# Optimization experiments

Hardware: AMD Instinct MI355X
Metric: run time of the kernel (lower is better)

Reference implementation:

```python
import jax, jax.numpy as jnp
import numpy as np

N_NODES = 100000
N_EDGES = 1600000
D_IN = 128
D_HID = 128
LATENT = 64
N_GRAPHS = 512


def setup_inputs() -> dict:
    key = jax.random.key(0)
    ks = jax.random.split(key, 10)
    x = jax.random.normal(ks[0], (N_NODES, D_IN), dtype=jnp.float32)
    edge_index = jax.random.randint(ks[1], (2, N_EDGES), 0, N_NODES, dtype=jnp.int64)
    batch = jnp.sort(jax.random.randint(ks[2], (N_NODES,), 0, N_GRAPHS, dtype=jnp.int64))
    def lin(k, fan_in, fan_out):
        return jax.random.normal(k, (fan_in, fan_out), dtype=jnp.float32) / np.sqrt(fan_in)
    W1 = lin(ks[3], D_IN, D_HID); b1 = jnp.zeros((D_HID,), jnp.float32)
    W2 = lin(ks[4], D_HID, D_HID); b2 = jnp.zeros((D_HID,), jnp.float32)
    W3 = lin(ks[5], D_HID, 2 * LATENT); b3 = jnp.zeros((2 * LATENT,), jnp.float32)
    return {"x": x, "edge_index": edge_index, "batch": batch,
            "W1": W1, "b1": b1, "W2": W2, "b2": b2, "W3": W3, "b3": b3}


def _gcn_norm(edge_index, n_nodes):
    # PyG GCNConv default: add self-loops, symmetric normalization
    loop = jnp.arange(n_nodes, dtype=edge_index.dtype)
    src = jnp.concatenate([edge_index[0], loop])
    dst = jnp.concatenate([edge_index[1], loop])
    deg = jax.ops.segment_sum(jnp.ones_like(dst, dtype=jnp.float32), dst,
                              num_segments=n_nodes)
    dinv = jnp.where(deg > 0, jax.lax.rsqrt(deg), 0.0)
    norm = dinv[src] * dinv[dst]  # [E + N]
    return src, dst, norm


def _gcn_conv(x, W, b, src, dst, norm, n_nodes):
    h = x @ W                               # [N, d_out]
    msg = h[src] * norm[:, None]            # gather + scale, [E+N, d_out]
    agg = jax.ops.segment_sum(msg, dst, num_segments=n_nodes)
    return agg + b


def reference(x, edge_index, batch, W1, b1, W2, b2, W3, b3):
    n = x.shape[0]
    src, dst, norm = _gcn_norm(edge_index, n)
    h = jax.nn.relu(_gcn_conv(x, W1, b1, src, dst, norm, n))
    h = jax.nn.relu(_gcn_conv(h, W2, b2, src, dst, norm, n))
    h = _gcn_conv(h, W3, b3, src, dst, norm, n)
    # scatter_mean over batch ids -> [num_graphs, 2*latent]
    cnt = jax.ops.segment_sum(jnp.ones((n,), jnp.float32), batch,
                              num_segments=N_GRAPHS)
    summed = jax.ops.segment_sum(h, batch, num_segments=N_GRAPHS)
    return summed / jnp.maximum(cnt, 1.0)[:, None]
```

## Files before the change

kernel.cpp:

```cpp
#include <hip/hip_runtime.h>
#include <stdint.h>

typedef unsigned short u16;
typedef unsigned int   u32;

#define N_NODES  100000
#define N_EDGES  1600000
#define DFEAT    128
#define N_GRAPHS 512

#define NBKT   391
#define EPB    8192
#define NBLK_E 196
#define LBUF   8192

typedef float f32x4 __attribute__((ext_vector_type(4)));
typedef short s16x8 __attribute__((ext_vector_type(8)));

__device__ __forceinline__ float bflo(u32 u) { return __uint_as_float(u << 16); }
__device__ __forceinline__ float bfhi(u32 u) { return __uint_as_float(u & 0xffff0000u); }
__device__ __forceinline__ u16 f2bf(float f) {
  u32 u = __float_as_uint(f);
  return (u16)((u + 0x7fffu + ((u >> 16) & 1u)) >> 16);
}
__device__ __forceinline__ u32 pack2(float f0, float f1) {
  return (u32)f2bf(f0) | ((u32)f2bf(f1) << 16);
}

__device__ __forceinline__ int ld_src(const int* ei, int m, int e) {
  return m ? ei[2 * e] : ei[e];
}
__device__ __forceinline__ int ld_dst(const int* ei, int m, int e) {
  return m ? ei[2 * (N_EDGES + e)] : ei[N_EDGES + e];
}

__device__ __forceinline__ int detect_m_block(const int* __restrict__ ei, int* sm) {
  int t = threadIdx.x;
  if (t < 64) {
    int v = ei[2 * t + 1];
    unsigned long long b = __ballot(v != 0);
    if (t == 0) *sm = (b == 0ull) ? 1 : 0;
  }
  __syncthreads();
  return *sm;
}

__global__ __launch_bounds__(256) void histA_k(const int* __restrict__ ei,
                                               int* __restrict__ ghist,
                                               const float* __restrict__ W1,
                                               const float* __restrict__ W2,
                                               const float* __restrict__ W3,
                                               u16* __restrict__ T1, u16* __restrict__ T2,
                                               u16* __restrict__ T3, int* __restrict__ flag) {
  int t = threadIdx.x, b = blockIdx.x;
  if (b >= NBLK_E) {
    int r = b - NBLK_E;
    if (r < 3) {
      const float* W = (r == 0) ? W1 : (r == 1) ? W2 : W3;
      u16* T         = (r == 0) ? T1 : (r == 1) ? T2 : T3;
      for (int i = t; i < DFEAT * DFEAT; i += 256) {
        int n = i >> 7, k = i & 127;
        T[i] = f2bf(W[k * DFEAT + n]);
      }
    } else {
      if (t < 64) {
        int v = ei[2 * t + 1];
        unsigned long long mm = __ballot(v != 0);
        if (t == 0) *flag = (mm == 0ull) ? 1 : 0;
      }
    }
    return;
  }
  __shared__ int sm;
  __shared__ int hist[NBKT];
  int m = detect_m_block(ei, &sm);
  for (int i = t; i < NBKT; i += 256) hist[i] = 0;
  __syncthreads();
  int e0 = b * EPB;
#pragma unroll
  for (int p = 0; p < EPB / 256; p++) {
    int e = e0 + p * 256 + t;
    if (e < N_EDGES) atomicAdd(&hist[ld_dst(ei, m, e) >> 8], 1);
  }
  __syncthreads();
  for (int i = t; i < NBKT; i += 256) ghist[b * NBKT + i] = hist[i];
}

__global__ __launch_bounds__(256) void scanB1_k(int* __restrict__ ghist,
                                                int* __restrict__ gtot) {
  __shared__ int ts[256];
  int t = threadIdx.x, k = blockIdx.x;
  int v = (t < NBLK_E) ? ghist[t * NBKT + k] : 0;
  ts[t] = v;
  for (int off = 1; off < 256; off <<= 1) {
    __syncthreads(); int add = (t >= off) ? ts[t - off] : 0;
    __syncthreads(); ts[t] += add;
  }
  __syncthreads();
  if (t < NBLK_E) ghist[t * NBKT + k] = ts[t] - v;
  if (t == 255) gtot[k] = ts[255];
}

__device__ __forceinline__ void scan_gtot_block(const int* __restrict__ gtot,
                                                int* bb, int* sc) {
  int t = threadIdx.x;
  int v0 = gtot[t];
  sc[t] = v0;
  for (int off = 1; off < 256; off <<= 1) {
    __syncthreads(); int add = (t >= off) ? sc[t - off] : 0;
    __syncthreads(); sc[t] += add;
  }
  __syncthreads();
  bb[t] = sc[t] - v0;
  int base256 = sc[255];
  __syncthreads();
  int v1 = (t < NBKT - 256) ? gtot[256 + t] : 0;
  sc[t] = v1;
  for (int off = 1; off < 256; off <<= 1) {
    __syncthreads(); int add = (t >= off) ? sc[t - off] : 0;
    __syncthreads(); sc[t] += add;
  }
  __syncthreads();
  if (t < NBKT - 256) bb[256 + t] = base256 + sc[t] - v1;
  if (t == 0) bb[NBKT] = N_EDGES;
  __syncthreads();
}

__global__ __launch_bounds__(256) void scatterC_k(const int* __restrict__ ei,
                                                  const int* __restrict__ obase,
                                                  const int* __restrict__ gtot,
                                                  u32* __restrict__ colpk) {
  __shared__ int sm;
  __shared__ int cur[NBKT];
  __shared__ int bb[NBKT + 1];
  __shared__ int sc[256];
  int t = threadIdx.x, b = blockIdx.x;
  int m = detect_m_block(ei, &sm);
  scan_gtot_block(gtot, bb, sc);
  for (int i = t; i < NBKT; i += 256) cur[i] = bb[i] + obase[b * NBKT + i];
  __syncthreads();
  int e0 = b * EPB;
#pragma unroll
  for (int p = 0; p < EPB / 256; p++) {
    int e = e0 + p * 256 + t;
    if (e < N_EDGES) {
      int d = ld_dst(ei, m, e);
      int s = ld_src(ei, m, e);
      int pos = atomicAdd(&cur[d >> 8], 1);
      colpk[pos] = (u32)s | ((u32)(d & 255) << 24);
    }
  }
}

__global__ __launch_bounds__(256) void fillD_k(const int* __restrict__ gtot,
                                               const u32* __restrict__ colpk,
                                               int* __restrict__ colarr,
                                               int* __restrict__ rowptr,
                                               float* __restrict__ dinv) {
  __shared__ int hist[256];
  __shared__ int cur[256];
  __shared__ int lbuf[LBUF];
  __shared__ int bb[NBKT + 1];
  __shared__ int sc[256];
  int t = threadIdx.x, b = blockIdx.x;
  scan_gtot_block(gtot, bb, sc);
  int base = bb[b], end = bb[b + 1], cnt = end - base;
  hist[t] = 0;
  __syncthreads();
  for (int i = t; i < cnt; i += 256) atomicAdd(&hist[colpk[base + i] >> 24], 1);
  __syncthreads();
  int c = hist[t];
  cur[t] = c;
  for (int off = 1; off < 256; off <<= 1) {
    __syncthreads(); int add = (t >= off) ? cur[t - off] : 0;
    __syncthreads(); cur[t] += add;
  }
  __syncthreads();
  int excl = cur[t] - c;
  int node = b * 256 + t;
  if (node < N_NODES) {
    rowptr[node] = base + excl;
    dinv[node] = rsqrtf((float)(c + 1));
  }
  if (b == NBKT - 1 && t == 0) rowptr[N_NODES] = N_EDGES;
  __syncthreads();
  cur[t] = excl;
  __syncthreads();
  for (int i = t; i < cnt; i += 256) {
    u32 v = colpk[base + i];
    int slot = atomicAdd(&cur[v >> 24], 1);
    if (slot < LBUF) lbuf[slot] = (int)(v & 0x00FFFFFFu);
  }
  __syncthreads();
  for (int i = t; i < cnt; i += 256) colarr[base + i] = lbuf[i];
}

#define LP 136

__global__ __launch_bounds__(256, 1) void gemm_scale_k(const void* __restrict__ Xv,
                                                       int x_is_f32,
                                                       const u16* __restrict__ Wt,
                                                       const float* __restrict__ dinv,
                                                       u16* __restrict__ Y, int nrows) {
  __shared__ u16 sX[128 * LP];
  __shared__ u16 sW[128 * LP];
  int tid = threadIdx.x;
  int r0 = blockIdx.x * 128;

  for (int c = tid; c < 2048; c += 256) {
    int row = c >> 4, off = (c & 15) * 8;
    *(uint4*)(&sW[row * LP + off]) = *(const uint4*)(Wt + row * DFEAT + off);
  }
  if (x_is_f32) {
    const float* Xf = (const float*)Xv;
    for (int c = tid; c < 2048; c += 256) {
      int row = c >> 4, off = (c & 15) * 8;
      int grow = r0 + row;
      uint4 o = make_uint4(0, 0, 0, 0);
      if (grow < nrows) {
        const float* px = Xf + (size_t)grow * DFEAT + off;
        float4 v0 = *(const float4*)px;
        float4 v1 = *(const float4*)(px + 4);
        o.x = pack2(v0.x, v0.y); o.y = pack2(v0.z, v0.w);
        o.z = pack2(v1.x, v1.y); o.w = pack2(v1.z, v1.w);
      }
      *(uint4*)(&sX[row * LP + off]) = o;
    }
  } else {
    const u16* Xb = (const u16*)Xv;
    for (int c = tid; c < 2048; c += 256) {
      int row = c >> 4, off = (c & 15) * 8;
      int grow = r0 + row;
      uint4 v = make_uint4(0, 0, 0, 0);
      if (grow < nrows) v = *(const uint4*)(Xb + (size_t)grow * DFEAT + off);
      *(uint4*)(&sX[row * LP + off]) = v;
    }
  }
  __syncthreads();

  int wave = tid >> 6, lane = tid & 63;
  int q = lane >> 4, r = lane & 15;
  int wr0 = wave * 32;

  f32x4 acc[2][8];
#pragma unroll
  for (int m = 0; m < 2; m++)
#pragma unroll
    for (int i = 0; i < 8; i++) acc[m][i] = (f32x4){0.f, 0.f, 0.f, 0.f};

#pragma unroll
  for (int kk = 0; kk < 4; kk++) {
    int k0 = kk * 32;
    s16x8 a0 = *(const s16x8*)(&sX[(wr0 + r) * LP + k0 + q * 8]);
    s16x8 a1 = *(const s16x8*)(&sX[(wr0 + 16 + r) * LP + k0 + q * 8]);
#pragma unroll
    for (int nt = 0; nt < 8; nt++) {
      s16x8 b = *(const s16x8*)(&sW[(nt * 16 + r) * LP + k0 + q * 8]);
      acc[0][nt] = __builtin_amdgcn_mfma_f32_16x16x32_bf16(a0, b, acc[0][nt], 0, 0, 0);
      acc[1][nt] = __builtin_amdgcn_mfma_f32_16x16x32_bf16(a1, b, acc[1][nt], 0, 0, 0);
    }
  }

#pragma unroll
  for (int m = 0; m < 2; m++) {
#pragma unroll
    for (int i = 0; i < 4; i++) {
      int grow = r0 + wr0 + m * 16 + q * 4 + i;
      if (grow < nrows) {
        float dv = dinv[grow];
#pragma unroll
        for (int nt = 0; nt < 8; nt++) {
          Y[(size_t)grow * DFEAT + nt * 16 + r] = f2bf(acc[m][nt][i] * dv);
        }
      }
    }
  }
}

struct Acc8 {
  float a0, a1, a2, a3, a4, a5, a6, a7;
  __device__ __forceinline__ void add(uint4 v) {
    a0 += bflo(v.x); a1 += bfhi(v.x); a2 += bflo(v.y); a3 += bfhi(v.y);
    a4 += bflo(v.z); a5 += bfhi(v.z); a6 += bflo(v.w); a7 += bfhi(v.w);
  }
};

__global__ __launch_bounds__(256) void agg_k(const u32* __restrict__ HS,
                                             const float* __restrict__ dinv,
                                             const int* __restrict__ rowptr,
                                             const int* __restrict__ colidx,
                                             const float* __restrict__ bias,
                                             u32* __restrict__ OUT, int do_relu) {
  int t = threadIdx.x;
  int node = blockIdx.x * 16 + (t >> 4);
  int fp = t & 15;

  int s = rowptr[node], e = rowptr[node + 1];

  Acc8 A;
  uint4 v = *(const uint4*)(HS + (size_t)node * 64 + fp * 4);
  A.a0 = bflo(v.x); A.a1 = bfhi(v.x); A.a2 = bflo(v.y); A.a3 = bfhi(v.y);
  A.a4 = bflo(v.z); A.a5 = bfhi(v.z); A.a6 = bflo(v.w); A.a7 = bfhi(v.w);

  int j = s;
  for (; j + 4 <= e; j += 4) {
    int i0 = colidx[j], i1 = colidx[j + 1], i2 = colidx[j + 2], i3 = colidx[j + 3];
    uint4 w0 = *(const uint4*)(HS + (size_t)i0 * 64 + fp * 4);
    uint4 w1 = *(const uint4*)(HS + (size_t)i1 * 64 + fp * 4);
    uint4 w2 = *(const uint4*)(HS + (size_t)i2 * 64 + fp * 4);
    uint4 w3 = *(const uint4*)(HS + (size_t)i3 * 64 + fp * 4);
    A.add(w0); A.add(w1); A.add(w2); A.add(w3);
  }
  for (; j < e; j++) {
    int i0 = colidx[j];
    uint4 w0 = *(const uint4*)(HS + (size_t)i0 * 64 + fp * 4);
    A.add(w0);
  }

  float dv = dinv[node];
  float4 b0 = *(const float4*)(bias + fp * 8);
  float4 b1 = *(const float4*)(bias + fp * 8 + 4);
  float r0 = A.a0 * dv + b0.x, r1 = A.a1 * dv + b0.y;
  float r2 = A.a2 * dv + b0.z, r3 = A.a3 * dv + b0.w;
  float r4 = A.a4 * dv + b1.x, r5 = A.a5 * dv + b1.y;
  float r6 = A.a6 * dv + b1.z, r7 = A.a7 * dv + b1.w;
  if (do_relu) {
    r0 = fmaxf(r0, 0.f); r1 = fmaxf(r1, 0.f); r2 = fmaxf(r2, 0.f); r3 = fmaxf(r3, 0.f);
    r4 = fmaxf(r4, 0.f); r5 = fmaxf(r5, 0.f); r6 = fmaxf(r6, 0.f); r7 = fmaxf(r7, 0.f);
  }
  uint4 o;
  o.x = pack2(r0, r1); o.y = pack2(r2, r3); o.z = pack2(r4, r5); o.w = pack2(r6, r7);
  *(uint4*)(OUT + (size_t)node * 64 + fp * 4) = o;
}

__device__ __forceinline__ int lower_bound_i(const int* a, int n, int key, int shift) {
  int lo = 0, hi = n;
  while (lo < hi) {
    int mid = (lo + hi) >> 1;
    if (a[mid << shift] < key) lo = mid + 1; else hi = mid;
  }
  return lo;
}

__global__ __launch_bounds__(256) void pool_k(const u32* __restrict__ H,
                                              const int* __restrict__ batch,
                                              const int* __restrict__ flag,
                                              float* __restrict__ OUT) {
  int g = blockIdx.x;
  int m = *flag;
  int lo = lower_bound_i(batch, N_NODES, g, m);
  int hi = lower_bound_i(batch, N_NODES, g + 1, m);
  int cnt = hi - lo;
  int d2 = threadIdx.x & 63;
  int half = threadIdx.x >> 6;
  float a0 = 0.f, a1 = 0.f;
  for (int row = lo + half; row < hi; row += 4) {
    u32 v = H[(size_t)row * 64 + d2];
    a0 += bflo(v); a1 += bfhi(v);
  }
  __shared__ float red0[256], red1[256];
  red0[threadIdx.x] = a0; red1[threadIdx.x] = a1;
  __syncthreads();
  if (threadIdx.x < 64) {
    float s0 = red0[d2] + red0[d2 + 64] + red0[d2 + 128] + red0[d2 + 192];
    float s1 = red1[d2] + red1[d2 + 64] + red1[d2 + 128] + red1[d2 + 192];
    float inv = 1.0f / fmaxf((float)cnt, 1.0f);
    OUT[g * DFEAT + 2 * d2]     = s0 * inv;
    OUT[g * DFEAT + 2 * d2 + 1] = s1 * inv;
  }
}


extern "C" void kernel_launch(void* const* d_in, const int* in_sizes, int n_in,
                              void* d_out, int out_size, void* d_ws, size_t ws_size,
                              hipStream_t stream) {
  const float* x   = (const float*)d_in[0];
  const int* ei    = (const int*)d_in[1];
  const int* batch = (const int*)d_in[2];
  const float* W1  = (const float*)d_in[3];
  const float* b1  = (const float*)d_in[4];
  const float* W2  = (const float*)d_in[5];
  const float* b2  = (const float*)d_in[6];
  const float* W3  = (const float*)d_in[7];
  const float* b3  = (const float*)d_in[8];
  float* out = (float*)d_out;

  char* p = (char*)d_ws;
  size_t off = 0;
  auto carve = [&](size_t bytes) -> void* {
    void* q = p + off;
    off = (off + bytes + 255) & ~(size_t)255;
    return q;
  };
  int*   flag   = (int*)carve(256);
  int*   ghist  = (int*)carve((size_t)NBLK_E * NBKT * 4);
  int*   gtot   = (int*)carve(NBKT * 4);
  int*   rowptr = (int*)carve((N_NODES + 1) * 4);
  float* dinv   = (float*)carve(N_NODES * 4);
  u32*   colpk  = (u32*)carve((size_t)N_EDGES * 4);
  int*   colarr = (int*)carve((size_t)N_EDGES * 4);
  u16*   Wt1    = (u16*)carve(DFEAT * DFEAT * 2);
  u16*   Wt2    = (u16*)carve(DFEAT * DFEAT * 2);
  u16*   Wt3    = (u16*)carve(DFEAT * DFEAT * 2);
  u32*   bufA   = (u32*)carve((size_t)N_NODES * 64 * 4);
  u32*   bufB   = (u32*)carve((size_t)N_NODES * 64 * 4);
  (void)ws_size;

  histA_k<<<NBLK_E + 4, 256, 0, stream>>>(ei, ghist, W1, W2, W3, Wt1, Wt2, Wt3, flag);
  scanB1_k<<<NBKT, 256, 0, stream>>>(ghist, gtot);
  scatterC_k<<<NBLK_E, 256, 0, stream>>>(ei, ghist, gtot, colpk);
  fillD_k<<<NBKT, 256, 0, stream>>>(gtot, colpk, colarr, rowptr, dinv);

  const int GB = (N_NODES + 127) / 128;
  const int AB = N_NODES / 16;

  gemm_scale_k<<<GB, 256, 0, stream>>>((const void*)x, 1, Wt1, dinv, (u16*)bufA, N_NODES);
  agg_k<<<AB, 256, 0, stream>>>(bufA, dinv, rowptr, colarr, b1, bufB, 1);
  gemm_scale_k<<<GB, 256, 0, stream>>>((const void*)bufB, 0, Wt2, dinv, (u16*)bufA, N_NODES);
  agg_k<<<AB, 256, 0, stream>>>(bufA, dinv, rowptr, colarr, b2, bufB, 1);
  gemm_scale_k<<<GB, 256, 0, stream>>>((const void*)bufB, 0, Wt3, dinv, (u16*)bufA, N_NODES);
  agg_k<<<AB, 256, 0, stream>>>(bufA, dinv, rowptr, colarr, b3, bufB, 0);
  pool_k<<<N_GRAPHS, 256, 0, stream>>>(bufB, batch, flag, out);
}
```

Before: 405.9 us.

## Fuse first GEMM with graph build and fuse aggregation with next-layer GEMM

The first-layer GEMM (with on-the-fly W1 transpose and bf16 conversion) now runs in the same launch as the edge histogram and weight prep, so it no longer waits on the CSR build. Because dinv is not yet known at that point, layer-1 aggregation applies the per-source dinv scaling inside the gather. Each aggregation is fused with the following layer's GEMM on a 16-row tile via MFMA, with weights read straight from global memory. The scan kernel is removed: scatter and fill blocks each re-sum the histogram columns redundantly. This cuts launches and intermediate round-trips, at the cost of redundant histogram reads, extra dinv gathers in layer 1, and a small-tile GEMM with poor weight reuse.

Result: slower. 436.9 us (+7.6%).

```diff
diff --git a/kernel.cpp b/kernel.cpp
--- a/kernel.cpp
+++ b/kernel.cpp
@@ -13,6 +13,7 @@
 #define EPB    8192
 #define NBLK_E 196
 #define LBUF   8192
+#define GB     782
 
 typedef float f32x4 __attribute__((ext_vector_type(4)));
 typedef short s16x8 __attribute__((ext_vector_type(8)));
@@ -45,66 +46,120 @@
   return *sm;
 }
 
-__global__ __launch_bounds__(256) void histA_k(const int* __restrict__ ei,
-                                               int* __restrict__ ghist,
-                                               const float* __restrict__ W1,
-                                               const float* __restrict__ W2,
-                                               const float* __restrict__ W3,
-                                               u16* __restrict__ T1, u16* __restrict__ T2,
-                                               u16* __restrict__ T3, int* __restrict__ flag) {
-  int t = threadIdx.x, b = blockIdx.x;
-  if (b >= NBLK_E) {
-    int r = b - NBLK_E;
-    if (r < 3) {
-      const float* W = (r == 0) ? W1 : (r == 1) ? W2 : W3;
-      u16* T         = (r == 0) ? T1 : (r == 1) ? T2 : T3;
-      for (int i = t; i < DFEAT * DFEAT; i += 256) {
-        int n = i >> 7, k = i & 127;
-        T[i] = f2bf(W[k * DFEAT + n]);
+#define LP 136
+
+__global__ __launch_bounds__(256) void mega_k(const float* __restrict__ x,
+                                              const int* __restrict__ ei,
+                                              int* __restrict__ ghist,
+                                              const float* __restrict__ W1,
+                                              const float* __restrict__ W2,
+                                              const float* __restrict__ W3,
+                                              u16* __restrict__ T2, u16* __restrict__ T3,
+                                              int* __restrict__ flag,
+                                              u16* __restrict__ Y) {
+  __shared__ u16 sX[128 * LP];
+  __shared__ u16 sW[128 * LP];
+  __shared__ int hist[NBKT];
+  __shared__ int sm;
+  int tid = threadIdx.x, b = blockIdx.x;
+
+  if (b < GB) {
+    int r0 = b * 128;
+    for (int c = tid; c < 2048; c += 256) {
+      int n = c & 127, k0 = (c >> 7) * 8;
+#pragma unroll
+      for (int j = 0; j < 8; j++)
+        sW[n * LP + k0 + j] = f2bf(W1[(size_t)(k0 + j) * DFEAT + n]);
+    }
+    for (int c = tid; c < 2048; c += 256) {
+      int row = c >> 4, off = (c & 15) * 8;
+      int grow = r0 + row;
+      uint4 o = make_uint4(0, 0, 0, 0);
+      if (grow < N_NODES) {
+        const float* px = x + (size_t)grow * DFEAT + off;
+        float4 v0 = *(const float4*)px;
+        float4 v1 = *(const float4*)(px + 4);
+        o.x = pack2(v0.x, v0.y); o.y = pack2(v0.z, v0.w);
+        o.z = pack2(v1.x, v1.y); o.w = pack2(v1.z, v1.w);
       }
-    } else {
-      if (t < 64) {
-        int v = ei[2 * t + 1];
-        unsigned long long mm = __ballot(v != 0);
-        if (t == 0) *flag = (mm == 0ull) ? 1 : 0;
+      *(uint4*)(&sX[row * LP + off]) = o;
+    }
+    __syncthreads();
+
+    int wave = tid >> 6, lane = tid & 63;
+    int q = lane >> 4, r = lane & 15;
+    int wr0 = wave * 32;
+
+    f32x4 acc[2][8];
+#pragma unroll
+    for (int m = 0; m < 2; m++)
+#pragma unroll
+      for (int i = 0; i < 8; i++) acc[m][i] = (f32x4){0.f, 0.f, 0.f, 0.f};
+
+#pragma unroll
+    for (int kk = 0; kk < 4; kk++) {
+      int k0 = kk * 32;
+      s16x8 a0 = *(const s16x8*)(&sX[(wr0 + r) * LP + k0 + q * 8]);
+      s16x8 a1 = *(const s16x8*)(&sX[(wr0 + 16 + r) * LP + k0 + q * 8]);
+#pragma unroll
+      for (int nt = 0; nt < 8; nt++) {
+        s16x8 bb = *(const s16x8*)(&sW[(nt * 16 + r) * LP + k0 + q * 8]);
+        acc[0][nt] = __builtin_amdgcn_mfma_f32_16x16x32_bf16(a0, bb, acc[0][nt], 0, 0, 0);
+        acc[1][nt] = __builtin_amdgcn_mfma_f32_16x16x32_bf16(a1, bb, acc[1][nt], 0, 0, 0);
       }
     }
+
+#pragma unroll
+    for (int m = 0; m < 2; m++) {
+#pragma unroll
+      for (int i = 0; i < 4; i++) {
+        int grow = r0 + wr0 + m * 16 + q * 4 + i;
+        if (grow < N_NODES) {
+#pragma unroll
+          for (int nt = 0; nt < 8; nt++)
+            Y[(size_t)grow * DFEAT + nt * 16 + r] = f2bf(acc[m][nt][i]);
+        }
+      }
+    }
     return;
   }
-  __shared__ int sm;
-  __shared__ int hist[NBKT];
-  int m = detect_m_block(ei, &sm);
-  for (int i = t; i < NBKT; i += 256) hist[i] = 0;
-  __syncthreads();
-  int e0 = b * EPB;
-#pragma unroll
-  for (int p = 0; p < EPB / 256; p++) {
-    int e = e0 + p * 256 + t;
-    if (e < N_EDGES) atomicAdd(&hist[ld_dst(ei, m, e) >> 8], 1);
-  }
-  __syncthreads();
-  for (int i = t; i < NBKT; i += 256) ghist[b * NBKT + i] = hist[i];
-}
-
-__global__ __launch_bounds__(256) void scanB1_k(int* __restrict__ ghist,
-                                                int* __restrict__ gtot) {
-  __shared__ int ts[256];
-  int t = threadIdx.x, k = blockIdx.x;
-  int v = (t < NBLK_E) ? ghist[t * NBKT + k] : 0;
-  ts[t] = v;
-  for (int off = 1; off < 256; off <<= 1) {
-    __syncthreads(); int add = (t >= off) ? ts[t - off] : 0;
-    __syncthreads(); ts[t] += add;
-  }
-  __syncthreads();
-  if (t < NBLK_E) ghist[t * NBKT + k] = ts[t] - v;
-  if (t == 255) gtot[k] = ts[255];
-}
-
-__device__ __forceinline__ void scan_gtot_block(const int* __restrict__ gtot,
-                                                int* bb, int* sc) {
+
+  if (b < GB + NBLK_E) {
+    int hb = b - GB;
+    int m = detect_m_block(ei, &sm);
+    for (int i = tid; i < NBKT; i += 256) hist[i] = 0;
+    __syncthreads();
+    int e0 = hb * EPB;
+#pragma unroll
+    for (int p = 0; p < EPB / 256; p++) {
+      int e = e0 + p * 256 + tid;
+      if (e < N_EDGES) atomicAdd(&hist[ld_dst(ei, m, e) >> 8], 1);
+    }
+    __syncthreads();
+    for (int i = tid; i < NBKT; i += 256) ghist[hb * NBKT + i] = hist[i];
+    return;
+  }
+
+  int r = b - GB - NBLK_E;
+  if (r < 2) {
+    const float* W = (r == 0) ? W2 : W3;
+    u16* T         = (r == 0) ? T2 : T3;
+    for (int i = tid; i < DFEAT * DFEAT; i += 256) {
+      int n = i >> 7, k = i & 127;
+      T[i] = f2bf(W[k * DFEAT + n]);
+    }
+  } else {
+    if (tid < 64) {
+      int v = ei[2 * tid + 1];
+      unsigned long long mm = __ballot(v != 0);
+      if (tid == 0) *flag = (mm == 0ull) ? 1 : 0;
+    }
+  }
+}
+
+__device__ __forceinline__ void scan_lds391(const int* arr, int* bb, int* sc) {
   int t = threadIdx.x;
-  int v0 = gtot[t];
+  int v0 = arr[t];
   sc[t] = v0;
   for (int off = 1; off < 256; off <<= 1) {
     __syncthreads(); int add = (t >= off) ? sc[t - off] : 0;
@@ -114,7 +169,7 @@
   bb[t] = sc[t] - v0;
   int base256 = sc[255];
   __syncthreads();
-  int v1 = (t < NBKT - 256) ? gtot[256 + t] : 0;
+  int v1 = (t < NBKT - 256) ? arr[256 + t] : 0;
   sc[t] = v1;
   for (int off = 1; off < 256; off <<= 1) {
     __syncthreads(); int add = (t >= off) ? sc[t - off] : 0;
@@ -127,17 +182,28 @@
 }
 
 __global__ __launch_bounds__(256) void scatterC_k(const int* __restrict__ ei,
-                                                  const int* __restrict__ obase,
-                                                  const int* __restrict__ gtot,
+                                                  const int* __restrict__ ghist,
                                                   u32* __restrict__ colpk) {
   __shared__ int sm;
+  __shared__ int colsum[NBKT];
+  __shared__ int colpre[NBKT];
   __shared__ int cur[NBKT];
   __shared__ int bb[NBKT + 1];
   __shared__ int sc[256];
   int t = threadIdx.x, b = blockIdx.x;
   int m = detect_m_block(ei, &sm);
-  scan_gtot_block(gtot, bb, sc);
-  for (int i = t; i < NBKT; i += 256) cur[i] = bb[i] + obase[b * NBKT + i];
+  for (int k = t; k < NBKT; k += 256) {
+    int tot = 0, pre = 0;
+    for (int b2 = 0; b2 < NBLK_E; b2++) {
+      int v = ghist[b2 * NBKT + k];
+      tot += v;
+      pre += (b2 < b) ? v : 0;
+    }
+    colsum[k] = tot; colpre[k] = pre;
+  }
+  __syncthreads();
+  scan_lds391(colsum, bb, sc);
+  for (int k = t; k < NBKT; k += 256) cur[k] = bb[k] + colpre[k];
   __syncthreads();
   int e0 = b * EPB;
 #pragma unroll
@@ -152,7 +218,7 @@
   }
 }
 
-__global__ __launch_bounds__(256) void fillD_k(const int* __restrict__ gtot,
+__global__ __launch_bounds__(256) void fillD_k(const int* __restrict__ ghist,
                                                const u32* __restrict__ colpk,
                                                int* __restrict__ colarr,
                                                int* __restrict__ rowptr,
@@ -160,10 +226,17 @@
   __shared__ int hist[256];
   __shared__ int cur[256];
   __shared__ int lbuf[LBUF];
+  __shared__ int colsum[NBKT];
   __shared__ int bb[NBKT + 1];
   __shared__ int sc[256];
   int t = threadIdx.x, b = blockIdx.x;
-  scan_gtot_block(gtot, bb, sc);
+  for (int k = t; k < NBKT; k += 256) {
+    int tot = 0;
+    for (int b2 = 0; b2 < NBLK_E; b2++) tot += ghist[b2 * NBKT + k];
+    colsum[k] = tot;
+  }
+  __syncthreads();
+  scan_lds391(colsum, bb, sc);
   int base = bb[b], end = bb[b + 1], cnt = end - base;
   hist[t] = 0;
   __syncthreads();
@@ -195,113 +268,28 @@
   for (int i = t; i < cnt; i += 256) colarr[base + i] = lbuf[i];
 }
 
-#define LP 136
-
-__global__ __launch_bounds__(256, 1) void gemm_scale_k(const void* __restrict__ Xv,
-                                                       int x_is_f32,
-                                                       const u16* __restrict__ Wt,
-                                                       const float* __restrict__ dinv,
-                                                       u16* __restrict__ Y, int nrows) {
-  __shared__ u16 sX[128 * LP];
-  __shared__ u16 sW[128 * LP];
-  int tid = threadIdx.x;
-  int r0 = blockIdx.x * 128;
-
-  for (int c = tid; c < 2048; c += 256) {
-    int row = c >> 4, off = (c & 15) * 8;
-    *(uint4*)(&sW[row * LP + off]) = *(const uint4*)(Wt + row * DFEAT + off);
-  }
-  if (x_is_f32) {
-    const float* Xf = (const float*)Xv;
-    for (int c = tid; c < 2048; c += 256) {
-      int row = c >> 4, off = (c & 15) * 8;
-      int grow = r0 + row;
-      uint4 o = make_uint4(0, 0, 0, 0);
-      if (grow < nrows) {
-        const float* px = Xf + (size_t)grow * DFEAT + off;
-        float4 v0 = *(const float4*)px;
-        float4 v1 = *(const float4*)(px + 4);
-        o.x = pack2(v0.x, v0.y); o.y = pack2(v0.z, v0.w);
-        o.z = pack2(v1.x, v1.y); o.w = pack2(v1.z, v1.w);
-      }
-      *(uint4*)(&sX[row * LP + off]) = o;
-    }
-  } else {
-    const u16* Xb = (const u16*)Xv;
-    for (int c = tid; c < 2048; c += 256) {
-      int row = c >> 4, off = (c & 15) * 8;
-      int grow = r0 + row;
-      uint4 v = make_uint4(0, 0, 0, 0);
-      if (grow < nrows) v = *(const uint4*)(Xb + (size_t)grow * DFEAT + off);
-      *(uint4*)(&sX[row * LP + off]) = v;
-    }
-  }
-  __syncthreads();
-
-  int wave = tid >> 6, lane = tid & 63;
-  int q = lane >> 4, r = lane & 15;
-  int wr0 = wave * 32;
-
-  f32x4 acc[2][8];
-#pragma unroll
-  for (int m = 0; m < 2; m++)
-#pragma unroll
-    for (int i = 0; i < 8; i++) acc[m][i] = (f32x4){0.f, 0.f, 0.f, 0.f};
-
-#pragma unroll
-  for (int kk = 0; kk < 4; kk++) {
-    int k0 = kk * 32;
-    s16x8 a0 = *(const s16x8*)(&sX[(wr0 + r) * LP + k0 + q * 8]);
-    s16x8 a1 = *(const s16x8*)(&sX[(wr0 + 16 + r) * LP + k0 + q * 8]);
-#pragma unroll
-    for (int nt = 0; nt < 8; nt++) {
-      s16x8 b = *(const s16x8*)(&sW[(nt * 16 + r) * LP + k0 + q * 8]);
-      acc[0][nt] = __builtin_amdgcn_mfma_f32_16x16x32_bf16(a0, b, acc[0][nt], 0, 0, 0);
-      acc[1][nt] = __builtin_amdgcn_mfma_f32_16x16x32_bf16(a1, b, acc[1][nt], 0, 0, 0);
-    }
-  }
-
-#pragma unroll
-  for (int m = 0; m < 2; m++) {
-#pragma unroll
-    for (int i = 0; i < 4; i++) {
-      int grow = r0 + wr0 + m * 16 + q * 4 + i;
-      if (grow < nrows) {
-        float dv = dinv[grow];
-#pragma unroll
-        for (int nt = 0; nt < 8; nt++) {
-          Y[(size_t)grow * DFEAT + nt * 16 + r] = f2bf(acc[m][nt][i] * dv);
-        }
-      }
-    }
-  }
-}
-
 struct Acc8 {
   float a0, a1, a2, a3, a4, a5, a6, a7;
-  __device__ __forceinline__ void add(uint4 v) {
+  __device__ __forceinline__ void zero() {
+    a0 = a1 = a2 = a3 = a4 = a5 = a6 = a7 = 0.f;
+  }
+  __device__ __forceinline__ void addv(uint4 v) {
     a0 += bflo(v.x); a1 += bfhi(v.x); a2 += bflo(v.y); a3 += bfhi(v.y);
     a4 += bflo(v.z); a5 += bfhi(v.z); a6 += bflo(v.w); a7 += bfhi(v.w);
   }
+  __device__ __forceinline__ void fmav(uint4 v, float s) {
+    a0 = fmaf(bflo(v.x), s, a0); a1 = fmaf(bfhi(v.x), s, a1);
+    a2 = fmaf(bflo(v.y), s, a2); a3 = fmaf(bfhi(v.y), s, a3);
+    a4 = fmaf(bflo(v.z), s, a4); a5 = fmaf(bfhi(v.z), s, a5);
+    a6 = fmaf(bflo(v.w), s, a6); a7 = fmaf(bfhi(v.w), s, a7);
+  }
 };
 
-__global__ __launch_bounds__(256) void agg_k(const u32* __restrict__ HS,
-                                             const float* __restrict__ dinv,
-                                             const int* __restrict__ rowptr,
-                                             const int* __restrict__ colidx,
-                                             const float* __restrict__ bias,
-                                             u32* __restrict__ OUT, int do_relu) {
-  int t = threadIdx.x;
-  int node = blockIdx.x * 16 + (t >> 4);
-  int fp = t & 15;
-
-  int s = rowptr[node], e = rowptr[node + 1];
-
-  Acc8 A;
-  uint4 v = *(const uint4*)(HS + (size_t)node * 64 + fp * 4);
-  A.a0 = bflo(v.x); A.a1 = bfhi(v.x); A.a2 = bflo(v.y); A.a3 = bfhi(v.y);
-  A.a4 = bflo(v.z); A.a5 = bfhi(v.z); A.a6 = bflo(v.w); A.a7 = bfhi(v.w);
-
+__device__ __forceinline__ Acc8 gather_plain(const u32* __restrict__ HS,
+                                             int s, int e, int node, int fp,
+                                             const int* __restrict__ colidx) {
+  Acc8 A; A.zero();
+  A.addv(*(const uint4*)(HS + (size_t)node * 64 + fp * 4));
   int j = s;
   for (; j + 4 <= e; j += 4) {
     int i0 = colidx[j], i1 = colidx[j + 1], i2 = colidx[j + 2], i3 = colidx[j + 3];
@@ -309,27 +297,114 @@
     uint4 w1 = *(const uint4*)(HS + (size_t)i1 * 64 + fp * 4);
     uint4 w2 = *(const uint4*)(HS + (size_t)i2 * 64 + fp * 4);
     uint4 w3 = *(const uint4*)(HS + (size_t)i3 * 64 + fp * 4);
-    A.add(w0); A.add(w1); A.add(w2); A.add(w3);
+    A.addv(w0); A.addv(w1); A.addv(w2); A.addv(w3);
+  }
+  for (; j < e; j++) {
+    A.addv(*(const uint4*)(HS + (size_t)colidx[j] * 64 + fp * 4));
+  }
+  return A;
+}
+
+__device__ __forceinline__ Acc8 gather_scaled(const u32* __restrict__ HS,
+                                              const float* __restrict__ dinv,
+                                              int s, int e, int node, int fp,
+                                              const int* __restrict__ colidx) {
+  Acc8 A; A.zero();
+  A.fmav(*(const uint4*)(HS + (size_t)node * 64 + fp * 4), dinv[node]);
+  int j = s;
+  for (; j + 4 <= e; j += 4) {
+    int i0 = colidx[j], i1 = colidx[j + 1], i2 = colidx[j + 2], i3 = colidx[j + 3];
+    float s0 = dinv[i0], s1 = dinv[i1], s2 = dinv[i2], s3 = dinv[i3];
+    uint4 w0 = *(const uint4*)(HS + (size_t)i0 * 64 + fp * 4);
+    uint4 w1 = *(const uint4*)(HS + (size_t)i1 * 64 + fp * 4);
+    uint4 w2 = *(const uint4*)(HS + (size_t)i2 * 64 + fp * 4);
+    uint4 w3 = *(const uint4*)(HS + (size_t)i3 * 64 + fp * 4);
+    A.fmav(w0, s0); A.fmav(w1, s1); A.fmav(w2, s2); A.fmav(w3, s3);
   }
   for (; j < e; j++) {
     int i0 = colidx[j];
-    uint4 w0 = *(const uint4*)(HS + (size_t)i0 * 64 + fp * 4);
-    A.add(w0);
-  }
+    A.fmav(*(const uint4*)(HS + (size_t)i0 * 64 + fp * 4), dinv[i0]);
+  }
+  return A;
+}
+
+__global__ __launch_bounds__(256) void aggmm_k(const u32* __restrict__ HS,
+                                               const float* __restrict__ dinv,
+                                               const int* __restrict__ rowptr,
+                                               const int* __restrict__ colidx,
+                                               const float* __restrict__ bias,
+                                               const u16* __restrict__ Wt,
+                                               u16* __restrict__ Y,
+                                               int src_scaled) {
+  __shared__ u16 sX[16 * LP];
+  int t = threadIdx.x;
+  int r0b = blockIdx.x * 16;
+  int lrow = t >> 4, fp = t & 15;
+  int node = r0b + lrow;
+  int s = rowptr[node], e = rowptr[node + 1];
+
+  Acc8 A;
+  if (src_scaled) A = gather_plain(HS, s, e, node, fp, colidx);
+  else            A = gather_scaled(HS, dinv, s, e, node, fp, colidx);
 
   float dv = dinv[node];
   float4 b0 = *(const float4*)(bias + fp * 8);
   float4 b1 = *(const float4*)(bias + fp * 8 + 4);
-  float r0 = A.a0 * dv + b0.x, r1 = A.a1 * dv + b0.y;
-  float r2 = A.a2 * dv + b0.z, r3 = A.a3 * dv + b0.w;
-  float r4 = A.a4 * dv + b1.x, r5 = A.a5 * dv + b1.y;
-  float r6 = A.a6 * dv + b1.z, r7 = A.a7 * dv + b1.w;
-  if (do_relu) {
-    r0 = fmaxf(r0, 0.f); r1 = fmaxf(r1, 0.f); r2 = fmaxf(r2, 0.f); r3 = fmaxf(r3, 0.f);
-    r4 = fmaxf(r4, 0.f); r5 = fmaxf(r5, 0.f); r6 = fmaxf(r6, 0.f); r7 = fmaxf(r7, 0.f);
-  }
+  float r0f = fmaxf(A.a0 * dv + b0.x, 0.f), r1f = fmaxf(A.a1 * dv + b0.y, 0.f);
+  float r2f = fmaxf(A.a2 * dv + b0.z, 0.f), r3f = fmaxf(A.a3 * dv + b0.w, 0.f);
+  float r4f = fmaxf(A.a4 * dv + b1.x, 0.f), r5f = fmaxf(A.a5 * dv + b1.y, 0.f);
+  float r6f = fmaxf(A.a6 * dv + b1.z, 0.f), r7f = fmaxf(A.a7 * dv + b1.w, 0.f);
   uint4 o;
-  o.x = pack2(r0, r1); o.y = pack2(r2, r3); o.z = pack2(r4, r5); o.w = pack2(r6, r7);
+  o.x = pack2(r0f, r1f); o.y = pack2(r2f, r3f);
+  o.z = pack2(r4f, r5f); o.w = pack2(r6f, r7f);
+  *(uint4*)(&sX[lrow * LP + fp * 8]) = o;
+  __syncthreads();
+
+  int wave = t >> 6, lane = t & 63;
+  int q = lane >> 4, r = lane & 15;
+  int nt0 = wave * 2, nt1 = wave * 2 + 1;
+
+  f32x4 acc0 = (f32x4){0.f, 0.f, 0.f, 0.f};
+  f32x4 acc1 = (f32x4){0.f, 0.f, 0.f, 0.f};
+#pragma unroll
+  for (int kk = 0; kk < 4; kk++) {
+    int k0 = kk * 32;
+    s16x8 a  = *(const s16x8*)(&sX[r * LP + k0 + q * 8]);
+    s16x8 w0 = *(const s16x8*)(Wt + (size_t)(nt0 * 16 + r) * DFEAT + k0 + q * 8);
+    s16x8 w1 = *(const s16x8*)(Wt + (size_t)(nt1 * 16 + r) * DFEAT + k0 + q * 8);
+    acc0 = __builtin_amdgcn_mfma_f32_16x16x32_bf16(a, w0, acc0, 0, 0, 0);
+    acc1 = __builtin_amdgcn_mfma_f32_16x16x32_bf16(a, w1, acc1, 0, 0, 0);
+  }
+#pragma unroll
+  for (int i = 0; i < 4; i++) {
+    int grow = r0b + q * 4 + i;
+    float dvv = dinv[grow];
+    Y[(size_t)grow * DFEAT + nt0 * 16 + r] = f2bf(acc0[i] * dvv);
+    Y[(size_t)grow * DFEAT + nt1 * 16 + r] = f2bf(acc1[i] * dvv);
+  }
+}
+
+__global__ __launch_bounds__(256) void agg_k(const u32* __restrict__ HS,
+                                             const float* __restrict__ dinv,
+                                             const int* __restrict__ rowptr,
+                                             const int* __restrict__ colidx,
+                                             const float* __restrict__ bias,
+                                             u32* __restrict__ OUT) {
+  int t = threadIdx.x;
+  int node = blockIdx.x * 16 + (t >> 4);
+  int fp = t & 15;
+  int s = rowptr[node], e = rowptr[node + 1];
+
+  Acc8 A = gather_plain(HS, s, e, node, fp, colidx);
+
+  float dv = dinv[node];
+  float4 b0 = *(const float4*)(bias + fp * 8);
+  float4 b1 = *(const float4*)(bias + fp * 8 + 4);
+  uint4 o;
+  o.x = pack2(A.a0 * dv + b0.x, A.a1 * dv + b0.y);
+  o.y = pack2(A.a2 * dv + b0.z, A.a3 * dv + b0.w);
+  o.z = pack2(A.a4 * dv + b1.x, A.a5 * dv + b1.y);
+  o.w = pack2(A.a6 * dv + b1.z, A.a7 * dv + b1.w);
   *(uint4*)(OUT + (size_t)node * 64 + fp * 4) = o;
 }
 
@@ -394,31 +469,24 @@
   };
   int*   flag   = (int*)carve(256);
   int*   ghist  = (int*)carve((size_t)NBLK_E * NBKT * 4);
-  int*   gtot   = (int*)carve(NBKT * 4);
   int*   rowptr = (int*)carve((N_NODES + 1) * 4);
   float* dinv   = (float*)carve(N_NODES * 4);
   u32*   colpk  = (u32*)carve((size_t)N_EDGES * 4);
   int*   colarr = (int*)carve((size_t)N_EDGES * 4);
-  u16*   Wt1    = (u16*)carve(DFEAT * DFEAT * 2);
   u16*   Wt2    = (u16*)carve(DFEAT * DFEAT * 2);
   u16*   Wt3    = (u16*)carve(DFEAT * DFEAT * 2);
   u32*   bufA   = (u32*)carve((size_t)N_NODES * 64 * 4);
   u32*   bufB   = (u32*)carve((size_t)N_NODES * 64 * 4);
   (void)ws_size;
 
-  histA_k<<<NBLK_E + 4, 256, 0, stream>>>(ei, ghist, W1, W2, W3, Wt1, Wt2, Wt3, flag);
-  scanB1_k<<<NBKT, 256, 0, stream>>>(ghist, gtot);
-  scatterC_k<<<NBLK_E, 256, 0, stream>>>(ei, ghist, gtot, colpk);
-  fillD_k<<<NBKT, 256, 0, stream>>>(gtot, colpk, colarr, rowptr, dinv);
-
-  const int GB = (N_NODES + 127) / 128;
   const int AB = N_NODES / 16;
 
-  gemm_scale_k<<<GB, 256, 0, stream>>>((const void*)x, 1, Wt1, dinv, (u16*)bufA, N_NODES);
-  agg_k<<<AB, 256, 0, stream>>>(bufA, dinv, rowptr, colarr, b1, bufB, 1);
-  gemm_scale_k<<<GB, 256, 0, stream>>>((const void*)bufB, 0, Wt2, dinv, (u16*)bufA, N_NODES);
-  agg_k<<<AB, 256, 0, stream>>>(bufA, dinv, rowptr, colarr, b2, bufB, 1);
-  gemm_scale_k<<<GB, 256, 0, stream>>>((const void*)bufB, 0, Wt3, dinv, (u16*)bufA, N_NODES);
-  agg_k<<<AB, 256, 0, stream>>>(bufA, dinv, rowptr, colarr, b3, bufB, 0);
+  mega_k<<<GB + NBLK_E + 3, 256, 0, stream>>>(x, ei, ghist, W1, W2, W3, Wt2, Wt3,
+                                              flag, (u16*)bufA);
+  scatterC_k<<<NBLK_E, 256, 0, stream>>>(ei, ghist, colpk);
+  fillD_k<<<NBKT, 256, 0, stream>>>(ghist, colpk, colarr, rowptr, dinv);
+  aggmm_k<<<AB, 256, 0, stream>>>(bufA, dinv, rowptr, colarr, b1, Wt2, (u16*)bufB, 0);
+  aggmm_k<<<AB, 256, 0, stream>>>(bufB, dinv, rowptr, colarr, b2, Wt3, (u16*)bufA, 1);
+  agg_k<<<AB, 256, 0, stream>>>(bufA, dinv, rowptr, colarr, b3, bufB);
   pool_k<<<N_GRAPHS, 256, 0, stream>>>(bufB, batch, flag, out);
 }
```

## Merge CSR build kernels into one cooperative kernel with grid syncs

Applied to the files above, without the earlier changes.

Replaces the four CSR-construction launches (histogram, column scan, scatter, per-bucket fill) with one cooperative kernel of 391 blocks that uses grid.sync between phases. The separate scan kernel is removed: every block now redundantly sums its column of the transposed histogram to get totals and its own prefix. This removes launch gaps and intermediate global round trips, at the cost of redundant per-block scan work, grid-wide barriers, and a large shared-memory footprint that must still allow all blocks to be co-resident.

After: 524.8 us. 1.29x slower.

```diff
diff --git a/kernel.cpp b/kernel.cpp
--- a/kernel.cpp
+++ b/kernel.cpp
@@ -1,5 +1,8 @@
 #include <hip/hip_runtime.h>
+#include <hip/hip_cooperative_groups.h>
 #include <stdint.h>
+
+namespace cg = cooperative_groups;
 
 typedef unsigned short u16;
 typedef unsigned int   u32;
@@ -45,138 +48,126 @@
   return *sm;
 }
 
-__global__ __launch_bounds__(256) void histA_k(const int* __restrict__ ei,
+__global__ __launch_bounds__(256) void build_k(const int* __restrict__ ei,
                                                int* __restrict__ ghist,
+                                               u32* __restrict__ colpk,
+                                               int* __restrict__ colarr,
+                                               int* __restrict__ rowptr,
+                                               float* __restrict__ dinv,
                                                const float* __restrict__ W1,
                                                const float* __restrict__ W2,
                                                const float* __restrict__ W3,
-                                               u16* __restrict__ T1, u16* __restrict__ T2,
-                                               u16* __restrict__ T3, int* __restrict__ flag) {
-  int t = threadIdx.x, b = blockIdx.x;
-  if (b >= NBLK_E) {
-    int r = b - NBLK_E;
-    if (r < 3) {
-      const float* W = (r == 0) ? W1 : (r == 1) ? W2 : W3;
-      u16* T         = (r == 0) ? T1 : (r == 1) ? T2 : T3;
-      for (int i = t; i < DFEAT * DFEAT; i += 256) {
-        int n = i >> 7, k = i & 127;
-        T[i] = f2bf(W[k * DFEAT + n]);
-      }
-    } else {
-      if (t < 64) {
-        int v = ei[2 * t + 1];
-        unsigned long long mm = __ballot(v != 0);
-        if (t == 0) *flag = (mm == 0ull) ? 1 : 0;
-      }
-    }
-    return;
-  }
+                                               u16* __restrict__ T1,
+                                               u16* __restrict__ T2,
+                                               u16* __restrict__ T3,
+                                               int* __restrict__ flag) {
+  cg::grid_group grid = cg::this_grid();
   __shared__ int sm;
   __shared__ int hist[NBKT];
-  int m = detect_m_block(ei, &sm);
-  for (int i = t; i < NBKT; i += 256) hist[i] = 0;
-  __syncthreads();
-  int e0 = b * EPB;
-#pragma unroll
-  for (int p = 0; p < EPB / 256; p++) {
-    int e = e0 + p * 256 + t;
-    if (e < N_EDGES) atomicAdd(&hist[ld_dst(ei, m, e) >> 8], 1);
-  }
-  __syncthreads();
-  for (int i = t; i < NBKT; i += 256) ghist[b * NBKT + i] = hist[i];
-}
-
-__global__ __launch_bounds__(256) void scanB1_k(int* __restrict__ ghist,
-                                                int* __restrict__ gtot) {
-  __shared__ int ts[256];
-  int t = threadIdx.x, k = blockIdx.x;
-  int v = (t < NBLK_E) ? ghist[t * NBKT + k] : 0;
-  ts[t] = v;
-  for (int off = 1; off < 256; off <<= 1) {
-    __syncthreads(); int add = (t >= off) ? ts[t - off] : 0;
-    __syncthreads(); ts[t] += add;
-  }
-  __syncthreads();
-  if (t < NBLK_E) ghist[t * NBKT + k] = ts[t] - v;
-  if (t == 255) gtot[k] = ts[255];
-}
-
-__device__ __forceinline__ void scan_gtot_block(const int* __restrict__ gtot,
-                                                int* bb, int* sc) {
-  int t = threadIdx.x;
-  int v0 = gtot[t];
-  sc[t] = v0;
-  for (int off = 1; off < 256; off <<= 1) {
-    __syncthreads(); int add = (t >= off) ? sc[t - off] : 0;
-    __syncthreads(); sc[t] += add;
-  }
-  __syncthreads();
-  bb[t] = sc[t] - v0;
-  int base256 = sc[255];
-  __syncthreads();
-  int v1 = (t < NBKT - 256) ? gtot[256 + t] : 0;
-  sc[t] = v1;
-  for (int off = 1; off < 256; off <<= 1) {
-    __syncthreads(); int add = (t >= off) ? sc[t - off] : 0;
-    __syncthreads(); sc[t] += add;
-  }
-  __syncthreads();
-  if (t < NBKT - 256) bb[256 + t] = base256 + sc[t] - v1;
-  if (t == 0) bb[NBKT] = N_EDGES;
-  __syncthreads();
-}
-
-__global__ __launch_bounds__(256) void scatterC_k(const int* __restrict__ ei,
-                                                  const int* __restrict__ obase,
-                                                  const int* __restrict__ gtot,
-                                                  u32* __restrict__ colpk) {
-  __shared__ int sm;
+  __shared__ int colsum[NBKT];
+  __shared__ int colpre[NBKT];
   __shared__ int cur[NBKT];
   __shared__ int bb[NBKT + 1];
   __shared__ int sc[256];
+  __shared__ int fhist[256];
+  __shared__ int fcur[256];
+  __shared__ int lbuf[LBUF];
+
   int t = threadIdx.x, b = blockIdx.x;
-  int m = detect_m_block(ei, &sm);
-  scan_gtot_block(gtot, bb, sc);
-  for (int i = t; i < NBKT; i += 256) cur[i] = bb[i] + obase[b * NBKT + i];
-  __syncthreads();
-  int e0 = b * EPB;
-#pragma unroll
-  for (int p = 0; p < EPB / 256; p++) {
-    int e = e0 + p * 256 + t;
-    if (e < N_EDGES) {
-      int d = ld_dst(ei, m, e);
-      int s = ld_src(ei, m, e);
-      int pos = atomicAdd(&cur[d >> 8], 1);
-      colpk[pos] = (u32)s | ((u32)(d & 255) << 24);
-    }
-  }
-}
-
-__global__ __launch_bounds__(256) void fillD_k(const int* __restrict__ gtot,
-                                               const u32* __restrict__ colpk,
-                                               int* __restrict__ colarr,
-                                               int* __restrict__ rowptr,
-                                               float* __restrict__ dinv) {
-  __shared__ int hist[256];
-  __shared__ int cur[256];
-  __shared__ int lbuf[LBUF];
-  __shared__ int bb[NBKT + 1];
-  __shared__ int sc[256];
-  int t = threadIdx.x, b = blockIdx.x;
-  scan_gtot_block(gtot, bb, sc);
+
+  if (b < NBLK_E) {
+    int m = detect_m_block(ei, &sm);
+    for (int i = t; i < NBKT; i += 256) hist[i] = 0;
+    __syncthreads();
+    int e0 = b * EPB;
+#pragma unroll
+    for (int p = 0; p < EPB / 256; p++) {
+      int e = e0 + p * 256 + t;
+      if (e < N_EDGES) atomicAdd(&hist[ld_dst(ei, m, e) >> 8], 1);
+    }
+    __syncthreads();
+    for (int i = t; i < NBKT; i += 256) ghist[(size_t)i * NBLK_E + b] = hist[i];
+  } else if (b < NBLK_E + 3) {
+    int r = b - NBLK_E;
+    const float* W = (r == 0) ? W1 : (r == 1) ? W2 : W3;
+    u16* T         = (r == 0) ? T1 : (r == 1) ? T2 : T3;
+    for (int i = t; i < DFEAT * DFEAT; i += 256) {
+      int n = i >> 7, k = i & 127;
+      T[i] = f2bf(W[k * DFEAT + n]);
+    }
+  } else if (b == NBLK_E + 3) {
+    if (t < 64) {
+      int v = ei[2 * t + 1];
+      unsigned long long mm = __ballot(v != 0);
+      if (t == 0) *flag = (mm == 0ull) ? 1 : 0;
+    }
+  }
+  grid.sync();
+
+  for (int k = t; k < NBKT; k += 256) {
+    const int* row = ghist + (size_t)k * NBLK_E;
+    int tot = 0, pre = 0;
+    for (int b2 = 0; b2 < NBLK_E; b2++) {
+      int v = row[b2];
+      tot += v;
+      pre += (b2 < b) ? v : 0;
+    }
+    colsum[k] = tot; colpre[k] = pre;
+  }
+  __syncthreads();
+  {
+    int v0 = colsum[t];
+    sc[t] = v0;
+    for (int off = 1; off < 256; off <<= 1) {
+      __syncthreads(); int add = (t >= off) ? sc[t - off] : 0;
+      __syncthreads(); sc[t] += add;
+    }
+    __syncthreads();
+    bb[t] = sc[t] - v0;
+    int base256 = sc[255];
+    __syncthreads();
+    int v1 = (t < NBKT - 256) ? colsum[256 + t] : 0;
+    sc[t] = v1;
+    for (int off = 1; off < 256; off <<= 1) {
+      __syncthreads(); int add = (t >= off) ? sc[t - off] : 0;
+      __syncthreads(); sc[t] += add;
+    }
+    __syncthreads();
+    if (t < NBKT - 256) bb[256 + t] = base256 + sc[t] - v1;
+    if (t == 0) bb[NBKT] = N_EDGES;
+    __syncthreads();
+  }
+  if (b < NBLK_E) {
+    int m = detect_m_block(ei, &sm);
+    for (int k = t; k < NBKT; k += 256) cur[k] = bb[k] + colpre[k];
+    __syncthreads();
+    int e0 = b * EPB;
+#pragma unroll
+    for (int p = 0; p < EPB / 256; p++) {
+      int e = e0 + p * 256 + t;
+      if (e < N_EDGES) {
+        int d = ld_dst(ei, m, e);
+        int s = ld_src(ei, m, e);
+        int pos = atomicAdd(&cur[d >> 8], 1);
+        colpk[pos] = (u32)s | ((u32)(d & 255) << 24);
+      }
+    }
+  }
+  grid.sync();
+
   int base = bb[b], end = bb[b + 1], cnt = end - base;
-  hist[t] = 0;
-  __syncthreads();
-  for (int i = t; i < cnt; i += 256) atomicAdd(&hist[colpk[base + i] >> 24], 1);
-  __syncthreads();
-  int c = hist[t];
-  cur[t] = c;
+  fhist[t] = 0;
+  __syncthreads();
+  for (int i = t; i < cnt; i += 256) atomicAdd(&fhist[colpk[base + i] >> 24], 1);
+  __syncthreads();
+  int c = fhist[t];
+  fcur[t] = c;
   for (int off = 1; off < 256; off <<= 1) {
-    __syncthreads(); int add = (t >= off) ? cur[t - off] : 0;
-    __syncthreads(); cur[t] += add;
-  }
-  __syncthreads();
-  int excl = cur[t] - c;
+    __syncthreads(); int add = (t >= off) ? fcur[t - off] : 0;
+    __syncthreads(); fcur[t] += add;
+  }
+  __syncthreads();
+  int excl = fcur[t] - c;
   int node = b * 256 + t;
   if (node < N_NODES) {
     rowptr[node] = base + excl;
@@ -184,11 +175,11 @@
   }
   if (b == NBKT - 1 && t == 0) rowptr[N_NODES] = N_EDGES;
   __syncthreads();
-  cur[t] = excl;
+  fcur[t] = excl;
   __syncthreads();
   for (int i = t; i < cnt; i += 256) {
     u32 v = colpk[base + i];
-    int slot = atomicAdd(&cur[v >> 24], 1);
+    int slot = atomicAdd(&fcur[v >> 24], 1);
     if (slot < LBUF) lbuf[slot] = (int)(v & 0x00FFFFFFu);
   }
   __syncthreads();
@@ -393,8 +384,7 @@
     return q;
   };
   int*   flag   = (int*)carve(256);
-  int*   ghist  = (int*)carve((size_t)NBLK_E * NBKT * 4);
-  int*   gtot   = (int*)carve(NBKT * 4);
+  int*   ghist  = (int*)carve((size_t)NBKT * NBLK_E * 4);
   int*   rowptr = (int*)carve((N_NODES + 1) * 4);
   float* dinv   = (float*)carve(N_NODES * 4);
   u32*   colpk  = (u32*)carve((size_t)N_EDGES * 4);
@@ -406,14 +396,16 @@
   u32*   bufB   = (u32*)carve((size_t)N_NODES * 64 * 4);
   (void)ws_size;
 
-  histA_k<<<NBLK_E + 4, 256, 0, stream>>>(ei, ghist, W1, W2, W3, Wt1, Wt2, Wt3, flag);
-  scanB1_k<<<NBKT, 256, 0, stream>>>(ghist, gtot);
-  scatterC_k<<<NBLK_E, 256, 0, stream>>>(ei, ghist, gtot, colpk);
-  fillD_k<<<NBKT, 256, 0, stream>>>(gtot, colpk, colarr, rowptr, dinv);
-
+  const int AB = N_NODES / 16;
   const int GB = (N_NODES + 127) / 128;
-  const int AB = N_NODES / 16;
-
+
+  {
+    void* kargs[] = {(void*)&ei, (void*)&ghist, (void*)&colpk, (void*)&colarr,
+                     (void*)&rowptr, (void*)&dinv, (void*)&W1, (void*)&W2,
+                     (void*)&W3, (void*)&Wt1, (void*)&Wt2, (void*)&Wt3,
+                     (void*)&flag};
+    hipLaunchCooperativeKernel((void*)build_k, dim3(NBKT), dim3(256), kargs, 0, stream);
+  }
   gemm_scale_k<<<GB, 256, 0, stream>>>((const void*)x, 1, Wt1, dinv, (u16*)bufA, N_NODES);
   agg_k<<<AB, 256, 0, stream>>>(bufA, dinv, rowptr, colarr, b1, bufB, 1);
   gemm_scale_k<<<GB, 256, 0, stream>>>((const void*)bufB, 0, Wt2, dinv, (u16*)bufA, N_NODES);
```
